# Kernel optimization log

Measured on AMD Instinct MI355X. Metric: run time of the kernel, lower is better.

The kernel has to match this reference:

```python
import jax, jax.numpy as jnp
import numpy as np

B, L, H = 2, 2048, 1536
I, N, R, K = 3072, 16, 96, 4


def setup_inputs() -> dict:
    key = jax.random.key(0)
    ks = jax.random.split(key, 10)
    rn = lambda k, shape, s: jax.random.normal(k, shape, jnp.float32) * s
    return {
        "hidden_states": rn(ks[0], (B, L, H), 1.0),
        "W_in": rn(ks[1], (2 * I, H), 0.02),
        "conv_w": rn(ks[2], (I, K), 0.1),
        "conv_b": rn(ks[3], (I,), 0.1),
        "W_x": rn(ks[4], (R + 2 * N, I), 0.02),
        "W_dt": rn(ks[5], (I, R), 0.02),
        "dt_bias": rn(ks[6], (I,), 0.1),
        # vLLM's weight loader stores A = -exp(A_log); replicate that here
        "A": -jnp.exp(rn(ks[7], (I, N), 0.5)),
        "D": jnp.ones((I,), jnp.float32),
        "W_out": rn(ks[8], (H, I), 0.02),
    }


def reference(hidden_states, W_in, conv_w, conv_b, W_x, W_dt, dt_bias, A, D, W_out):
    b, l, _ = hidden_states.shape
    k = conv_w.shape[1]
    n = A.shape[1]
    r = W_dt.shape[1]

    # in_proj -> [B,L,2I], split into ssm input x and gate
    proj = jnp.einsum("blh,eh->ble", hidden_states, W_in)
    x, gate = jnp.split(proj, 2, axis=-1)  # each [B,L,I]

    # causal depthwise conv1d over L (pad K-1 on the left) + SiLU
    xp = jnp.pad(x, ((0, 0), (k - 1, 0), (0, 0)))
    conv = sum(xp[:, j : j + l, :] * conv_w[:, j] for j in range(k)) + conv_b
    x = jax.nn.silu(conv)  # [B,L,I]

    # x_proj -> dt (rank R), B, C (each N)
    ssm_p = jnp.einsum("bli,pi->blp", x, W_x)
    dt_in, Bm, Cm = jnp.split(ssm_p, [r, r + n], axis=-1)

    # dt_proj (skip_bias_add) then softplus(dt + bias) inside the scan math
    dt = jnp.einsum("blr,ir->bli", dt_in, W_dt)
    delta = jax.nn.softplus(dt + dt_bias)  # [B,L,I]

    # selective scan: s_t = exp(delta_t * A) * s_{t-1} + delta_t * x_t * B_t
    def step(state, inp):
        d_t, u_t, B_t, C_t = inp  # [B,I], [B,I], [B,N], [B,N]
        dA = jnp.exp(d_t[..., None] * A)  # [B,I,N]
        state = state * dA + (d_t * u_t)[..., None] * B_t[:, None, :]
        y = jnp.einsum("bin,bn->bi", state, C_t)
        return state, y

    init = jnp.zeros((b, x.shape[-1], n), jnp.float32)
    _, ys = jax.lax.scan(
        step,
        init,
        (
            delta.transpose(1, 0, 2),
            x.transpose(1, 0, 2),
            Bm.transpose(1, 0, 2),
            Cm.transpose(1, 0, 2),
        ),
    )
    y = ys.transpose(1, 0, 2) + x * D  # skip connection via D
    y = y * jax.nn.silu(gate)

    # out_proj -> [B,L,H]
    return jnp.einsum("bli,hi->blh", y, W_out)
```

## Files before the change

kernel.cpp:

```cpp
#include <hip/hip_runtime.h>

typedef __attribute__((ext_vector_type(8))) short bf16x8;
typedef __attribute__((ext_vector_type(4))) float f32x4;

#define CCH 32
#define TCH 64

__device__ __forceinline__ unsigned short f2b(float f) {
    unsigned u = __float_as_uint(f);
    return (unsigned short)((u + 0x7fffu + ((u >> 16) & 1u)) >> 16);
}
__device__ __forceinline__ float b2f(unsigned short h) {
    return __uint_as_float(((unsigned)h) << 16);
}
__device__ __forceinline__ float softplus_f(float z) {
    return (z > 15.f) ? z : __logf(1.f + __expf(z));
}
__device__ __forceinline__ float silu_f(float g) {
    return g / (1.f + __expf(-g));
}

__device__ __forceinline__ void gload16(const unsigned short* g, unsigned short* l) {
    __builtin_amdgcn_global_load_lds(
        (const __attribute__((address_space(1))) void*)g,
        (__attribute__((address_space(3))) void*)l, 16, 0, 0);
}

__global__ __launch_bounds__(256)
void cast_all(const float* __restrict__ h, const float* __restrict__ win,
              const float* __restrict__ wx, const float* __restrict__ wdt,
              const float* __restrict__ wout,
              unsigned short* __restrict__ dh, unsigned short* __restrict__ dwin,
              unsigned short* __restrict__ dwx, unsigned short* __restrict__ dwdt,
              unsigned short* __restrict__ dwout) {
    const int n0 = 1572864, n1 = n0 + 2359296, n2 = n1 + 98304,
              n3 = n2 + 73728, n4 = n3 + 1179648;
    int i = blockIdx.x * 256 + threadIdx.x;
    const float* s; unsigned short* d; int off;
    if (i < n0)      { s = h;    d = dh;    off = i; }
    else if (i < n1) { s = win;  d = dwin;  off = i - n0; }
    else if (i < n2) { s = wx;   d = dwx;   off = i - n1; }
    else if (i < n3) { s = wdt;  d = dwdt;  off = i - n2; }
    else if (i < n4) { s = wout; d = dwout; off = i - n3; }
    else return;
    float4 v = reinterpret_cast<const float4*>(s)[off];
    ushort4 o;
    o.x = f2b(v.x); o.y = f2b(v.y); o.z = f2b(v.z); o.w = f2b(v.w);
    reinterpret_cast<ushort4*>(d)[off] = o;
}

__global__ __launch_bounds__(768, 3)
void gemm_in(const unsigned short* __restrict__ A, const unsigned short* __restrict__ W,
             unsigned short* __restrict__ Cout, int Kc, int lda, int ldw, int ldc,
             int silu_col0) {
    __shared__ __align__(16) unsigned short A0s[8192];
    __shared__ __align__(16) unsigned short B0s[12288];
    __shared__ __align__(16) unsigned short A1s[8192];
    __shared__ __align__(16) unsigned short B1s[12288];
    const int tid  = threadIdx.x;
    const int lane = tid & 63;
    const int wave = tid >> 6;
    const int wr   = wave / 6;
    const int wcc  = wave % 6;
    const int lr   = lane & 15;
    const int quad = lane >> 4;
    const int sw2  = (lr >> 1) & 3;

    const int c  = blockIdx.x & 7;
    const int j  = blockIdx.x >> 3;
    const int bn = (c * 2 + (j & 1)) * 384;
    const int bm = (j >> 1) * 256;

    const int rsub = wave * 16 + (lane >> 2);
    const int csw  = ((lane & 3) ^ ((lane >> 3) & 3)) * 8;
    const unsigned short* gA = A + (size_t)(bm + rsub) * lda + csw;
    const unsigned short* gB = W + (size_t)(bn + rsub) * ldw + csw;

#define STAGE_A(ARR, kt) do { \
        gload16(gA + (kt) * 32, ARR + wave * 512); \
        if (wave < 4) gload16(gA + (size_t)192 * lda + (kt) * 32, ARR + 6144 + wave * 512); \
    } while (0)
#define STAGE_B(ARR, kt) do { \
        gload16(gB + (kt) * 32, ARR + wave * 512); \
        gload16(gB + (size_t)192 * ldw + (kt) * 32, ARR + 6144 + wave * 512); \
    } while (0)

#define LDA_F(ARR, mi) \
    (*reinterpret_cast<const bf16x8*>(&ARR[(wr * 128 + (mi) * 16 + lr) * 32 + ((quad ^ sw2)) * 8]))
#define LDB_F(ARR, ni) \
    (*reinterpret_cast<const bf16x8*>(&ARR[(wcc * 64 + (ni) * 16 + lr) * 32 + ((quad ^ sw2)) * 8]))

#define PRIO1 __builtin_amdgcn_s_setprio(1)
#define PRIO0 __builtin_amdgcn_s_setprio(0)
#define VM0B  asm volatile("s_waitcnt vmcnt(0)\n\ts_barrier" ::: "memory")

#define TILE_BODY(AX, BX) do { \
        _Pragma("unroll") for (int ni = 0; ni < 4; ++ni) fb[ni] = LDB_F(BX, ni); \
        _Pragma("unroll") for (int mp = 0; mp < 4; ++mp) { \
            bf16x8 fa0 = LDA_F(AX, 2 * mp); \
            bf16x8 fa1 = LDA_F(AX, 2 * mp + 1); \
            PRIO1; \
            _Pragma("unroll") for (int ni = 0; ni < 4; ++ni) { \
                acc[2 * mp][ni]     = __builtin_amdgcn_mfma_f32_16x16x32_bf16(fa0, fb[ni], acc[2 * mp][ni], 0, 0, 0); \
                acc[2 * mp + 1][ni] = __builtin_amdgcn_mfma_f32_16x16x32_bf16(fa1, fb[ni], acc[2 * mp + 1][ni], 0, 0, 0); } \
            PRIO0; } \
    } while (0)

    f32x4 acc[8][4];
    const f32x4 zero = {0.f, 0.f, 0.f, 0.f};
#pragma unroll
    for (int m = 0; m < 8; ++m)
#pragma unroll
        for (int n = 0; n < 4; ++n) acc[m][n] = zero;

    bf16x8 fb[4];

    const int nkt = Kc >> 5;

    STAGE_A(A0s, 0); STAGE_B(B0s, 0);
    VM0B;

#pragma unroll 1
    for (int t = 0; t < nkt; t += 2) {
        if (t + 1 < nkt) { STAGE_A(A1s, t + 1); STAGE_B(B1s, t + 1); }
        TILE_BODY(A0s, B0s);
        VM0B;
        if (t + 1 < nkt) {
            if (t + 2 < nkt) { STAGE_A(A0s, t + 2); STAGE_B(B0s, t + 2); }
            TILE_BODY(A1s, B1s);
            VM0B;
        }
    }

#pragma unroll
    for (int mi = 0; mi < 8; ++mi) {
        const int row0 = bm + wr * 128 + mi * 16 + quad * 4;
#pragma unroll
        for (int ni = 0; ni < 4; ++ni) {
            const int col = bn + wcc * 64 + ni * 16 + lr;
#pragma unroll
            for (int reg = 0; reg < 4; ++reg) {
                float v = acc[mi][ni][reg];
                if (col >= silu_col0) v = silu_f(v);
                Cout[(size_t)(row0 + reg) * ldc + col] = f2b(v);
            }
        }
    }
#undef STAGE_A
#undef STAGE_B
#undef LDA_F
#undef LDB_F
#undef PRIO1
#undef PRIO0
#undef VM0B
#undef TILE_BODY
}

__global__ __launch_bounds__(768, 3)
void gemm_out(const unsigned short* __restrict__ A, const unsigned short* __restrict__ W,
              float* __restrict__ Cout, int Kc, int lda, int ldw, int ldc) {
    __shared__ __align__(16) unsigned short A0s[8192];
    __shared__ __align__(16) unsigned short B0s[12288];
    __shared__ __align__(16) unsigned short A1s[8192];
    __shared__ __align__(16) unsigned short B1s[12288];
    const int tid  = threadIdx.x;
    const int lane = tid & 63;
    const int wave = tid >> 6;
    const int wr   = wave / 6;
    const int wcc  = wave % 6;
    const int lr   = lane & 15;
    const int quad = lane >> 4;
    const int sw   = lr & 7;

    const int c  = blockIdx.x & 7;
    const int j  = blockIdx.x >> 3;
    const int bm = j * 128;
    const int bn = c * 192;

    const int rsub = wave * 8 + (lane >> 3);
    const int csw  = ((lane & 7) ^ ((lane >> 3) & 7)) * 8;
    const unsigned short* gA = A + (size_t)(bm + rsub) * lda + csw;
    const unsigned short* gB = W + (size_t)(bn + rsub) * ldw + csw;

#define STAGE_A(ARR, kt) do { \
        gload16(gA + (kt) * 64, ARR + wave * 512); \
        if (wave < 4) gload16(gA + (size_t)96 * lda + (kt) * 64, ARR + 6144 + wave * 512); \
    } while (0)
#define STAGE_B(ARR, kt) do { \
        gload16(gB + (kt) * 64, ARR + wave * 512); \
        gload16(gB + (size_t)96 * ldw + (kt) * 64, ARR + 6144 + wave * 512); \
    } while (0)

#define LDA_F(ARR, mi, kk) \
    (*reinterpret_cast<const bf16x8*>(&ARR[(wr * 64 + (mi) * 16 + lr) * 64 + (((((kk) << 2) | quad)) ^ sw) * 8]))
#define LDB_F(ARR, ni, kk) \
    (*reinterpret_cast<const bf16x8*>(&ARR[(wcc * 32 + (ni) * 16 + lr) * 64 + (((((kk) << 2) | quad)) ^ sw) * 8]))

#define PRIO1 __builtin_amdgcn_s_setprio(1)
#define PRIO0 __builtin_amdgcn_s_setprio(0)
#define VM0B  asm volatile("s_waitcnt vmcnt(0)\n\ts_barrier" ::: "memory")

#define TILE_BODY(AX, BX) do { \
        _Pragma("unroll") for (int ni = 0; ni < 2; ++ni) { \
            fb[ni][0] = LDB_F(BX, ni, 0); fb[ni][1] = LDB_F(BX, ni, 1); } \
        _Pragma("unroll") for (int mi = 0; mi < 4; ++mi) { \
            fa[mi][0] = LDA_F(AX, mi, 0); fa[mi][1] = LDA_F(AX, mi, 1); } \
        PRIO1; \
        _Pragma("unroll") for (int mi = 0; mi < 4; ++mi) \
        _Pragma("unroll") for (int ni = 0; ni < 2; ++ni) { \
            acc[mi][ni] = __builtin_amdgcn_mfma_f32_16x16x32_bf16(fa[mi][0], fb[ni][0], acc[mi][ni], 0, 0, 0); \
            acc[mi][ni] = __builtin_amdgcn_mfma_f32_16x16x32_bf16(fa[mi][1], fb[ni][1], acc[mi][ni], 0, 0, 0); } \
        PRIO0; \
    } while (0)

    f32x4 acc[4][2];
    const f32x4 zero = {0.f, 0.f, 0.f, 0.f};
#pragma unroll
    for (int m = 0; m < 4; ++m) { acc[m][0] = zero; acc[m][1] = zero; }

    bf16x8 fa[4][2], fb[2][2];

    const int nkt = Kc >> 6;

    STAGE_A(A0s, 0); STAGE_B(B0s, 0);
    VM0B;

#pragma unroll 1
    for (int t = 0; t < nkt; t += 2) {
        if (t + 1 < nkt) { STAGE_A(A1s, t + 1); STAGE_B(B1s, t + 1); }
        TILE_BODY(A0s, B0s);
        VM0B;
        if (t + 1 < nkt) {
            if (t + 2 < nkt) { STAGE_A(A0s, t + 2); STAGE_B(B0s, t + 2); }
            TILE_BODY(A1s, B1s);
            VM0B;
        }
    }

#pragma unroll
    for (int mi = 0; mi < 4; ++mi) {
        const int row0 = bm + wr * 64 + mi * 16 + quad * 4;
#pragma unroll
        for (int ni = 0; ni < 2; ++ni) {
            const int col = bn + wcc * 32 + ni * 16 + lr;
#pragma unroll
            for (int reg = 0; reg < 4; ++reg)
                Cout[(size_t)(row0 + reg) * ldc + col] = acc[mi][ni][reg];
        }
    }
#undef STAGE_A
#undef STAGE_B
#undef LDA_F
#undef LDB_F
#undef PRIO1
#undef PRIO0
#undef VM0B
#undef TILE_BODY
}

template <int OP>
__global__ __launch_bounds__(256)
void gemm_mfma(const unsigned short* __restrict__ A, const unsigned short* __restrict__ W,
               void* __restrict__ Cout, int Kc, int lda, int ldw, int ldc,
               const float* __restrict__ bias, int silu_col0, long long czs) {
    __shared__ unsigned short As[3][4096];
    __shared__ unsigned short Bs[3][4096];
    const int tid = threadIdx.x;
    const int bm = blockIdx.y * 128;
    const int bn = blockIdx.x * 128;
    const int kz = blockIdx.z;
    A += (size_t)kz * Kc;
    W += (size_t)kz * Kc;
    const int lane = tid & 63;
    const int wave = tid >> 6;
    const int r_a = lane >> 2;
    const int k8 = (lane & 3) * 8;

    const unsigned short* gA0 = A + (size_t)(bm + wave * 16 + r_a) * lda + k8;
    const unsigned short* gA1 = A + (size_t)(bm + 64 + wave * 16 + r_a) * lda + k8;
    const unsigned short* gB0 = W + (size_t)(bn + wave * 16 + r_a) * ldw + k8;
    const unsigned short* gB1 = W + (size_t)(bn + 64 + wave * 16 + r_a) * ldw + k8;

    const int wm = (wave & 1) * 64;
    const int wn = (wave >> 1) * 64;
    const int lr = lane & 15;
    const int quad = lane >> 4;

    f32x4 acc[4][4];
    const f32x4 zero = {0.f, 0.f, 0.f, 0.f};
#pragma unroll
    for (int i = 0; i < 4; i++)
#pragma unroll
        for (int j = 0; j < 4; j++) acc[i][j] = zero;

#define STAGE(koff, j) do { \
        gload16(gA0 + (koff), As[j] + wave * 512); \
        gload16(gA1 + (koff), As[j] + (wave + 4) * 512); \
        gload16(gB0 + (koff), Bs[j] + wave * 512); \
        gload16(gB1 + (koff), Bs[j] + (wave + 4) * 512); \
    } while (0)

    const int niter = Kc >> 5;
    STAGE(0, 0);
    if (niter > 1) STAGE(32, 1);

    int ib = 0;
    for (int k = 0; k < niter; k++) {
        if (k + 1 < niter)
            asm volatile("s_waitcnt vmcnt(4)\n\ts_barrier" ::: "memory");
        else
            asm volatile("s_waitcnt vmcnt(0)\n\ts_barrier" ::: "memory");
        if (k + 2 < niter) {
            int is_ = ib + 2; if (is_ >= 3) is_ -= 3;
            STAGE((k + 2) << 5, is_);
        }
        const unsigned short* as = As[ib];
        const unsigned short* bs = Bs[ib];
        bf16x8 fa[4], fb[4];
#pragma unroll
        for (int mi = 0; mi < 4; mi++)
            fa[mi] = *reinterpret_cast<const bf16x8*>(as + (wm + mi * 16 + lr) * 32 + quad * 8);
#pragma unroll
        for (int ni = 0; ni < 4; ni++)
            fb[ni] = *reinterpret_cast<const bf16x8*>(bs + (wn + ni * 16 + lr) * 32 + quad * 8);
#pragma unroll
        for (int mi = 0; mi < 4; mi++)
#pragma unroll
            for (int ni = 0; ni < 4; ni++)
                acc[mi][ni] = __builtin_amdgcn_mfma_f32_16x16x32_bf16(fa[mi], fb[ni], acc[mi][ni], 0, 0, 0);
        ib = (ib == 2) ? 0 : ib + 1;
    }
#undef STAGE

#pragma unroll
    for (int mi = 0; mi < 4; mi++)
#pragma unroll
        for (int reg = 0; reg < 4; reg++) {
            int row = bm + wm + mi * 16 + quad * 4 + reg;
#pragma unroll
            for (int ni = 0; ni < 4; ni++) {
                int col = bn + wn + ni * 16 + lr;
                float v = acc[mi][ni][reg];
                if (OP == 0) {
                    float* Cf = (float*)Cout + (size_t)kz * czs;
                    Cf[(size_t)row * ldc + col] = v;
                } else if (OP == 2) {
                    if (col >= silu_col0) v = silu_f(v);
                    ((unsigned short*)Cout)[(size_t)row * ldc + col] = f2b(v);
                } else {
                    ((unsigned short*)Cout)[(size_t)row * ldc + col] = f2b(softplus_f(v + bias[col]));
                }
            }
        }
}

__global__ __launch_bounds__(256)
void reduce_xpart(const float* __restrict__ xpart, float* __restrict__ ssmp,
                  unsigned short* __restrict__ dtin) {
    const int BL = 4096;
    int idx = blockIdx.x * 256 + threadIdx.x;
    int row = idx >> 5;
    int c4 = (idx & 31) * 4;
    float4 s = {0.f, 0.f, 0.f, 0.f};
#pragma unroll
    for (int z = 0; z < 8; z++) {
        float4 v = *reinterpret_cast<const float4*>(xpart + (size_t)z * BL * 128 + (size_t)row * 128 + c4);
        s.x += v.x; s.y += v.y; s.z += v.z; s.w += v.w;
    }
    *reinterpret_cast<float4*>(ssmp + (size_t)row * 128 + c4) = s;
    if (c4 < 96) {
        ushort4 o;
        o.x = f2b(s.x); o.y = f2b(s.y); o.z = f2b(s.z); o.w = f2b(s.w);
        *reinterpret_cast<ushort4*>(dtin + (size_t)row * 96 + c4) = o;
    }
}

__global__ __launch_bounds__(256)
void conv_silu8(const unsigned short* __restrict__ projbf, const float* __restrict__ cw,
                const float* __restrict__ cb, unsigned short* __restrict__ xc) {
    const int I = 3072, L = 2048, LD = 6144;
    int idx = blockIdx.x * 256 + threadIdx.x;
    int i8 = (idx % (I / 8)) * 8;
    int bl = idx / (I / 8);
    int l = bl & (L - 1);
    float s[8];
    {
        float4 b0 = *reinterpret_cast<const float4*>(cb + i8);
        float4 b1 = *reinterpret_cast<const float4*>(cb + i8 + 4);
        s[0]=b0.x; s[1]=b0.y; s[2]=b0.z; s[3]=b0.w; s[4]=b1.x; s[5]=b1.y; s[6]=b1.z; s[7]=b1.w;
    }
    float w[8][4];
#pragma unroll
    for (int c = 0; c < 8; c++) {
        float4 wr = *reinterpret_cast<const float4*>(cw + (i8 + c) * 4);
        w[c][0]=wr.x; w[c][1]=wr.y; w[c][2]=wr.z; w[c][3]=wr.w;
    }
#pragma unroll
    for (int j = 0; j < 4; j++) {
        if (l + j - 3 >= 0) {
            uint4 r = *reinterpret_cast<const uint4*>(projbf + (size_t)(bl + j - 3) * LD + i8);
            float xv[8];
            xv[0]=b2f((unsigned short)(r.x & 0xffff)); xv[1]=b2f((unsigned short)(r.x >> 16));
            xv[2]=b2f((unsigned short)(r.y & 0xffff)); xv[3]=b2f((unsigned short)(r.y >> 16));
            xv[4]=b2f((unsigned short)(r.z & 0xffff)); xv[5]=b2f((unsigned short)(r.z >> 16));
            xv[6]=b2f((unsigned short)(r.w & 0xffff)); xv[7]=b2f((unsigned short)(r.w >> 16));
#pragma unroll
            for (int c = 0; c < 8; c++) s[c] = fmaf(xv[c], w[c][j], s[c]);
        }
    }
    unsigned short o[8];
#pragma unroll
    for (int c = 0; c < 8; c++) o[c] = f2b(silu_f(s[c]));
    uint4 packed;
    packed.x = (unsigned)o[0] | ((unsigned)o[1] << 16);
    packed.y = (unsigned)o[2] | ((unsigned)o[3] << 16);
    packed.z = (unsigned)o[4] | ((unsigned)o[5] << 16);
    packed.w = (unsigned)o[6] | ((unsigned)o[7] << 16);
    *reinterpret_cast<uint4*>(xc + (size_t)bl * I + i8) = packed;
}

__global__ __launch_bounds__(256)
void scan_passA(const unsigned short* __restrict__ delta_bf, const unsigned short* __restrict__ xc,
                const float* __restrict__ ssmp, const float* __restrict__ Aw,
                float* __restrict__ S_local, float* __restrict__ sumDelta) {
    const int I = 3072, L = 2048;
    __shared__ float bc[TCH][32];
    int g = blockIdx.x * 256 + threadIdx.x;
    int i = g % I;
    int bcid = g / I;
    int c = bcid % CCH;
    int b = bcid / CCH;
    size_t rowbase = (size_t)b * L + (size_t)c * TCH;
    for (int e = threadIdx.x; e < TCH * 8; e += 256) {
        int t = e >> 3, q = e & 7;
        float4 v = *reinterpret_cast<const float4*>(ssmp + (rowbase + t) * 128 + 96 + q * 4);
        *reinterpret_cast<float4*>(&bc[t][q * 4]) = v;
    }
    __syncthreads();

    float Arow[16];
#pragma unroll
    for (int n = 0; n < 16; n++) Arow[n] = Aw[i * 16 + n];
    float st[16];
#pragma unroll
    for (int n = 0; n < 16; n++) st[n] = 0.f;
    float sumD = 0.f;

    size_t rowI = rowbase * I + i;
    for (int t = 0; t < TCH; t++) {
        float delta = b2f(delta_bf[rowI]);
        float du = delta * b2f(xc[rowI]);
        sumD += delta;
        float4 b0 = *reinterpret_cast<const float4*>(&bc[t][0]);
        float4 b1 = *reinterpret_cast<const float4*>(&bc[t][4]);
        float4 b2 = *reinterpret_cast<const float4*>(&bc[t][8]);
        float4 b3 = *reinterpret_cast<const float4*>(&bc[t][12]);
        const float bv[16] = {b0.x,b0.y,b0.z,b0.w, b1.x,b1.y,b1.z,b1.w,
                              b2.x,b2.y,b2.z,b2.w, b3.x,b3.y,b3.z,b3.w};
#pragma unroll
        for (int n = 0; n < 16; n++)
            st[n] = fmaf(st[n], __expf(delta * Arow[n]), du * bv[n]);
        rowI += I;
    }
    size_t obase = (size_t)bcid * 16 * I + i;
#pragma unroll
    for (int n = 0; n < 16; n++) S_local[obase + (size_t)n * I] = st[n];
    sumDelta[(size_t)bcid * I + i] = sumD;
}

__global__ __launch_bounds__(256)
void scan_passB(const float* __restrict__ S_local, const float* __restrict__ sumDelta,
                const float* __restrict__ Aw, float* __restrict__ state_in) {
    const int I = 3072;
    int g = blockIdx.x * 256 + threadIdx.x;
    int i = g % I;
    int bn = g / I;
    int n = bn & 15;
    int b = bn >> 4;
    float a = Aw[i * 16 + n];
    float state = 0.f;
    for (int c = 0; c < CCH; c++) {
        int bcid = b * CCH + c;
        size_t idx = ((size_t)bcid * 16 + n) * I + i;
        state_in[idx] = state;
        state = fmaf(state, __expf(a * sumDelta[(size_t)bcid * I + i]), S_local[idx]);
    }
}

__global__ __launch_bounds__(256)
void scan_passC(const unsigned short* __restrict__ projbf,
                const unsigned short* __restrict__ xc,
                const float* __restrict__ ssmp, const unsigned short* __restrict__ delta_bf,
                const float* __restrict__ Aw, const float* __restrict__ Dw,
                const float* __restrict__ state_in, unsigned short* __restrict__ ybf) {
    const int I = 3072, L = 2048, LD = 6144;
    __shared__ float bc[TCH][32];
    int g = blockIdx.x * 256 + threadIdx.x;
    int i = g % I;
    int bcid = g / I;
    int c = bcid % CCH;
    int b = bcid / CCH;
    size_t rowbase = (size_t)b * L + (size_t)c * TCH;
    for (int e = threadIdx.x; e < TCH * 8; e += 256) {
        int t = e >> 3, q = e & 7;
        float4 v = *reinterpret_cast<const float4*>(ssmp + (rowbase + t) * 128 + 96 + q * 4);
        *reinterpret_cast<float4*>(&bc[t][q * 4]) = v;
    }
    __syncthreads();

    float Arow[16];
#pragma unroll
    for (int n = 0; n < 16; n++) Arow[n] = Aw[i * 16 + n];
    float Dv = Dw[i];
    float st[16];
    size_t sbase = (size_t)bcid * 16 * I + i;
#pragma unroll
    for (int n = 0; n < 16; n++) st[n] = state_in[sbase + (size_t)n * I];

    size_t rowI = rowbase * I + i;
    size_t rowG = rowbase * LD + I + i;
    for (int t = 0; t < TCH; t++) {
        float delta = b2f(delta_bf[rowI]);
        float u = b2f(xc[rowI]);
        float du = delta * u;
        float4 b0 = *reinterpret_cast<const float4*>(&bc[t][0]);
        float4 b1 = *reinterpret_cast<const float4*>(&bc[t][4]);
        float4 b2 = *reinterpret_cast<const float4*>(&bc[t][8]);
        float4 b3 = *reinterpret_cast<const float4*>(&bc[t][12]);
        float4 c0 = *reinterpret_cast<const float4*>(&bc[t][16]);
        float4 c1 = *reinterpret_cast<const float4*>(&bc[t][20]);
        float4 c2 = *reinterpret_cast<const float4*>(&bc[t][24]);
        float4 c3 = *reinterpret_cast<const float4*>(&bc[t][28]);
        const float bv[16] = {b0.x,b0.y,b0.z,b0.w, b1.x,b1.y,b1.z,b1.w,
                              b2.x,b2.y,b2.z,b2.w, b3.x,b3.y,b3.z,b3.w};
        const float cv[16] = {c0.x,c0.y,c0.z,c0.w, c1.x,c1.y,c1.z,c1.w,
                              c2.x,c2.y,c2.z,c2.w, c3.x,c3.y,c3.z,c3.w};
        float y = 0.f;
#pragma unroll
        for (int n = 0; n < 16; n++) {
            st[n] = fmaf(st[n], __expf(delta * Arow[n]), du * bv[n]);
            y = fmaf(st[n], cv[n], y);
        }
        y = fmaf(u, Dv, y);
        y *= b2f(projbf[rowG]);
        ybf[rowI] = f2b(y);
        rowI += I;
        rowG += LD;
    }
}

extern "C" void kernel_launch(void* const* d_in, const int* in_sizes, int n_in,
                              void* d_out, int out_size, void* d_ws, size_t ws_size,
                              hipStream_t stream) {
    const float* hidden  = (const float*)d_in[0];
    const float* W_in    = (const float*)d_in[1];
    const float* conv_w  = (const float*)d_in[2];
    const float* conv_b  = (const float*)d_in[3];
    const float* W_x     = (const float*)d_in[4];
    const float* W_dt    = (const float*)d_in[5];
    const float* dt_bias = (const float*)d_in[6];
    const float* Aw      = (const float*)d_in[7];
    const float* Dw      = (const float*)d_in[8];
    const float* W_out   = (const float*)d_in[9];
    float* out = (float*)d_out;

    constexpr int Bsz = 2, L = 2048, H = 1536, I = 3072, R = 96;
    constexpr int BL = Bsz * L;
    constexpr int TwoI = 2 * I;

    char* base = (char*)d_ws;
    unsigned short* proj_bf  = (unsigned short*)base; base += (size_t)BL * TwoI * 2;
    unsigned short* delta_bf = (unsigned short*)base; base += (size_t)BL * I * 2;
    unsigned short* xc_bf    = (unsigned short*)base; base += (size_t)BL * I * 2;
    unsigned short* y_bf     = (unsigned short*)base; base += (size_t)BL * I * 2;
    float* ssmp              = (float*)base;          base += (size_t)BL * 128 * 4;
    float* xpart             = (float*)base;          base += (size_t)8 * BL * 128 * 4;
    unsigned short* dtin_bf  = (unsigned short*)base; base += (size_t)BL * R * 2;
    unsigned short* wx_bf    = (unsigned short*)base; base += (size_t)128 * I * 2;
    unsigned short* wdt_bf   = (unsigned short*)base; base += (size_t)I * R * 2;
    unsigned short* wout_bf  = (unsigned short*)base; base += (size_t)H * I * 2;
    unsigned short* h_bf     = (unsigned short*)base; base += (size_t)BL * H * 2;
    unsigned short* win_bf   = (unsigned short*)base; base += (size_t)TwoI * H * 2;
    float* S_local  = (float*)h_bf;
    float* sumDelta = S_local + (size_t)Bsz * CCH * 16 * I;
    float* state_in = sumDelta + (size_t)Bsz * CCH * I;

    dim3 blk(256);

    cast_all<<<(5283840 + 255) / 256, blk, 0, stream>>>(
        hidden, W_in, W_x, W_dt, W_out, h_bf, win_bf, wx_bf, wdt_bf, wout_bf);

    gemm_in<<<dim3(256, 1, 1), dim3(768), 0, stream>>>(
        h_bf, win_bf, proj_bf, H, H, H, TwoI,  I);

    conv_silu8<<<BL * I / 8 / 256, blk, 0, stream>>>(proj_bf, conv_w, conv_b, xc_bf);

    gemm_mfma<0><<<dim3(1, BL / 128, 8), blk, 0, stream>>>(
        xc_bf, wx_bf, xpart, I / 8, I, I, 128, nullptr, 0, (long long)BL * 128);
    reduce_xpart<<<BL * 32 / 256, blk, 0, stream>>>(xpart, ssmp, dtin_bf);

    gemm_mfma<3><<<dim3(I / 128, BL / 128, 1), blk, 0, stream>>>(
        dtin_bf, wdt_bf, delta_bf, R, R, R, I, dt_bias, 0, 0);

    scan_passA<<<Bsz * I * CCH / 256, blk, 0, stream>>>(
        delta_bf, xc_bf, ssmp, Aw, S_local, sumDelta);
    scan_passB<<<Bsz * 16 * I / 256, blk, 0, stream>>>(
        S_local, sumDelta, Aw, state_in);
    scan_passC<<<Bsz * I * CCH / 256, blk, 0, stream>>>(
        proj_bf, xc_bf, ssmp, delta_bf, Aw, Dw, state_in, y_bf);

    gemm_out<<<dim3(256, 1, 1), dim3(768), 0, stream>>>(
        y_bf, wout_bf, out, I, I, I, H);
}
```

Baseline: 450.1 us.

## Triple-buffer LDS tiles in in/out projection GEMMs with partial vmcnt waits

Both large bf16 GEMM kernels go from double to triple buffering of the A/B tiles in LDS. The main loop is restructured into three rotating slots, and each slot waits only for the older stage using per-wave vmcnt counts (4 or 3 loads, depending on whether the wave issues the extra A load), instead of draining all loads each iteration. This keeps two tile loads in flight to hide global-memory latency behind MFMA work. In exchange, LDS use per block grows by half, which can reduce how many blocks fit per CU. The loop also always executes three tile bodies per iteration, which assumes the K-tile count is a multiple of three.

```diff
diff --git a/kernel.cpp b/kernel.cpp
--- a/kernel.cpp
+++ b/kernel.cpp
@@ -54,9 +54,11 @@
              unsigned short* __restrict__ Cout, int Kc, int lda, int ldw, int ldc,
              int silu_col0) {
     __shared__ __align__(16) unsigned short A0s[8192];
+    __shared__ __align__(16) unsigned short A1s[8192];
+    __shared__ __align__(16) unsigned short A2s[8192];
     __shared__ __align__(16) unsigned short B0s[12288];
-    __shared__ __align__(16) unsigned short A1s[8192];
     __shared__ __align__(16) unsigned short B1s[12288];
+    __shared__ __align__(16) unsigned short B2s[12288];
     const int tid  = threadIdx.x;
     const int lane = tid & 63;
     const int wave = tid >> 6;
@@ -65,6 +67,7 @@
     const int lr   = lane & 15;
     const int quad = lane >> 4;
     const int sw2  = (lr >> 1) & 3;
+    const int hiAu = __builtin_amdgcn_readfirstlane(wave < 4 ? 1 : 0);
 
     const int c  = blockIdx.x & 7;
     const int j  = blockIdx.x >> 3;
@@ -78,7 +81,7 @@
 
 #define STAGE_A(ARR, kt) do { \
         gload16(gA + (kt) * 32, ARR + wave * 512); \
-        if (wave < 4) gload16(gA + (size_t)192 * lda + (kt) * 32, ARR + 6144 + wave * 512); \
+        if (hiAu) gload16(gA + (size_t)192 * lda + (kt) * 32, ARR + 6144 + wave * 512); \
     } while (0)
 #define STAGE_B(ARR, kt) do { \
         gload16(gB + (kt) * 32, ARR + wave * 512); \
@@ -92,7 +95,11 @@
 
 #define PRIO1 __builtin_amdgcn_s_setprio(1)
 #define PRIO0 __builtin_amdgcn_s_setprio(0)
-#define VM0B  asm volatile("s_waitcnt vmcnt(0)\n\ts_barrier" ::: "memory")
+#define WTB do { \
+        if (hiAu) asm volatile("s_waitcnt vmcnt(4)\n\ts_barrier" ::: "memory"); \
+        else      asm volatile("s_waitcnt vmcnt(3)\n\ts_barrier" ::: "memory"); \
+    } while (0)
+#define VM0B asm volatile("s_waitcnt vmcnt(0)\n\ts_barrier" ::: "memory")
 
 #define TILE_BODY(AX, BX) do { \
         _Pragma("unroll") for (int ni = 0; ni < 4; ++ni) fb[ni] = LDB_F(BX, ni); \
@@ -106,6 +113,14 @@
             PRIO0; } \
     } while (0)
 
+#define SLOT(RA, RB, SA, SB, ts) do { \
+        if ((ts) < nkt) { STAGE_A(SA, ts); STAGE_B(SB, ts); } \
+        TILE_BODY(RA, RB); \
+        if ((ts) < nkt)       WTB; \
+        else if ((ts) == nkt) VM0B; \
+        else asm volatile("s_barrier" ::: "memory"); \
+    } while (0)
+
     f32x4 acc[8][4];
     const f32x4 zero = {0.f, 0.f, 0.f, 0.f};
 #pragma unroll
@@ -118,18 +133,14 @@
     const int nkt = Kc >> 5;
 
     STAGE_A(A0s, 0); STAGE_B(B0s, 0);
-    VM0B;
+    STAGE_A(A1s, 1); STAGE_B(B1s, 1);
+    WTB;
 
 #pragma unroll 1
-    for (int t = 0; t < nkt; t += 2) {
-        if (t + 1 < nkt) { STAGE_A(A1s, t + 1); STAGE_B(B1s, t + 1); }
-        TILE_BODY(A0s, B0s);
-        VM0B;
-        if (t + 1 < nkt) {
-            if (t + 2 < nkt) { STAGE_A(A0s, t + 2); STAGE_B(B0s, t + 2); }
-            TILE_BODY(A1s, B1s);
-            VM0B;
-        }
+    for (int t = 0; t < nkt; t += 3) {
+        SLOT(A0s, B0s, A2s, B2s, t + 2);
+        SLOT(A1s, B1s, A0s, B0s, t + 3);
+        SLOT(A2s, B2s, A1s, B1s, t + 4);
     }
 
 #pragma unroll
@@ -152,17 +163,21 @@
 #undef LDB_F
 #undef PRIO1
 #undef PRIO0
+#undef WTB
 #undef VM0B
 #undef TILE_BODY
+#undef SLOT
 }
 
 __global__ __launch_bounds__(768, 3)
 void gemm_out(const unsigned short* __restrict__ A, const unsigned short* __restrict__ W,
               float* __restrict__ Cout, int Kc, int lda, int ldw, int ldc) {
     __shared__ __align__(16) unsigned short A0s[8192];
+    __shared__ __align__(16) unsigned short A1s[8192];
+    __shared__ __align__(16) unsigned short A2s[8192];
     __shared__ __align__(16) unsigned short B0s[12288];
-    __shared__ __align__(16) unsigned short A1s[8192];
     __shared__ __align__(16) unsigned short B1s[12288];
+    __shared__ __align__(16) unsigned short B2s[12288];
     const int tid  = threadIdx.x;
     const int lane = tid & 63;
     const int wave = tid >> 6;
@@ -171,6 +186,7 @@
     const int lr   = lane & 15;
     const int quad = lane >> 4;
     const int sw   = lr & 7;
+    const int hiAu = __builtin_amdgcn_readfirstlane(wave < 4 ? 1 : 0);
 
     const int c  = blockIdx.x & 7;
     const int j  = blockIdx.x >> 3;
@@ -184,7 +200,7 @@
 
 #define STAGE_A(ARR, kt) do { \
         gload16(gA + (kt) * 64, ARR + wave * 512); \
-        if (wave < 4) gload16(gA + (size_t)96 * lda + (kt) * 64, ARR + 6144 + wave * 512); \
+        if (hiAu) gload16(gA + (size_t)96 * lda + (kt) * 64, ARR + 6144 + wave * 512); \
     } while (0)
 #define STAGE_B(ARR, kt) do { \
         gload16(gB + (kt) * 64, ARR + wave * 512); \
@@ -198,7 +214,11 @@
 
 #define PRIO1 __builtin_amdgcn_s_setprio(1)
 #define PRIO0 __builtin_amdgcn_s_setprio(0)
-#define VM0B  asm volatile("s_waitcnt vmcnt(0)\n\ts_barrier" ::: "memory")
+#define WTB do { \
+        if (hiAu) asm volatile("s_waitcnt vmcnt(4)\n\ts_barrier" ::: "memory"); \
+        else      asm volatile("s_waitcnt vmcnt(3)\n\ts_barrier" ::: "memory"); \
+    } while (0)
+#define VM0B asm volatile("s_waitcnt vmcnt(0)\n\ts_barrier" ::: "memory")
 
 #define TILE_BODY(AX, BX) do { \
         _Pragma("unroll") for (int ni = 0; ni < 2; ++ni) { \
@@ -213,6 +233,14 @@
         PRIO0; \
     } while (0)
 
+#define SLOT(RA, RB, SA, SB, ts) do { \
+        if ((ts) < nkt) { STAGE_A(SA, ts); STAGE_B(SB, ts); } \
+        TILE_BODY(RA, RB); \
+        if ((ts) < nkt)       WTB; \
+        else if ((ts) == nkt) VM0B; \
+        else asm volatile("s_barrier" ::: "memory"); \
+    } while (0)
+
     f32x4 acc[4][2];
     const f32x4 zero = {0.f, 0.f, 0.f, 0.f};
 #pragma unroll
@@ -223,18 +251,14 @@
     const int nkt = Kc >> 6;
 
     STAGE_A(A0s, 0); STAGE_B(B0s, 0);
-    VM0B;
+    STAGE_A(A1s, 1); STAGE_B(B1s, 1);
+    WTB;
 
 #pragma unroll 1
-    for (int t = 0; t < nkt; t += 2) {
-        if (t + 1 < nkt) { STAGE_A(A1s, t + 1); STAGE_B(B1s, t + 1); }
-        TILE_BODY(A0s, B0s);
-        VM0B;
-        if (t + 1 < nkt) {
-            if (t + 2 < nkt) { STAGE_A(A0s, t + 2); STAGE_B(B0s, t + 2); }
-            TILE_BODY(A1s, B1s);
-            VM0B;
-        }
+    for (int t = 0; t < nkt; t += 3) {
+        SLOT(A0s, B0s, A2s, B2s, t + 2);
+        SLOT(A1s, B1s, A0s, B0s, t + 3);
+        SLOT(A2s, B2s, A1s, B1s, t + 4);
     }
 
 #pragma unroll
@@ -254,8 +278,10 @@
 #undef LDB_F
 #undef PRIO1
 #undef PRIO0
+#undef WTB
 #undef VM0B
 #undef TILE_BODY
+#undef SLOT
 }
 
 template <int OP>
```

Result: slower. 474.5 us (+5.4%).

## Triple-buffer the in-projection GEMM LDS pipeline with partial vmcnt waits

Applied to the files above, without the earlier changes.

The in-projection GEMM changes from a double-buffered LDS pipeline to a triple-buffered one. Loads for tile t+2 are issued while tile t is computed, and the wait becomes vmcnt(5), so only the older tile's loads must land before the barrier. Staging is reassigned so 8 of the 12 waves each issue 5 global-to-LDS loads, and the K loop is unrolled by three slots. The goal is to hide global-load latency better. The cost is 50% more LDS per block, which may reduce blocks resident per CU, and four idle waves during staging.

```diff
diff --git a/kernel.cpp b/kernel.cpp
--- a/kernel.cpp
+++ b/kernel.cpp
@@ -54,9 +54,11 @@
              unsigned short* __restrict__ Cout, int Kc, int lda, int ldw, int ldc,
              int silu_col0) {
     __shared__ __align__(16) unsigned short A0s[8192];
+    __shared__ __align__(16) unsigned short A1s[8192];
+    __shared__ __align__(16) unsigned short A2s[8192];
     __shared__ __align__(16) unsigned short B0s[12288];
-    __shared__ __align__(16) unsigned short A1s[8192];
     __shared__ __align__(16) unsigned short B1s[12288];
+    __shared__ __align__(16) unsigned short B2s[12288];
     const int tid  = threadIdx.x;
     const int lane = tid & 63;
     const int wave = tid >> 6;
@@ -71,18 +73,20 @@
     const int bn = (c * 2 + (j & 1)) * 384;
     const int bm = (j >> 1) * 256;
 
-    const int rsub = wave * 16 + (lane >> 2);
     const int csw  = ((lane & 3) ^ ((lane >> 3) & 3)) * 8;
-    const unsigned short* gA = A + (size_t)(bm + rsub) * lda + csw;
-    const unsigned short* gB = W + (size_t)(bn + rsub) * ldw + csw;
-
-#define STAGE_A(ARR, kt) do { \
-        gload16(gA + (kt) * 32, ARR + wave * 512); \
-        if (wave < 4) gload16(gA + (size_t)192 * lda + (kt) * 32, ARR + 6144 + wave * 512); \
-    } while (0)
-#define STAGE_B(ARR, kt) do { \
-        gload16(gB + (kt) * 32, ARR + wave * 512); \
-        gload16(gB + (size_t)192 * ldw + (kt) * 32, ARR + 6144 + wave * 512); \
+    const unsigned short* gAl = A + (size_t)(bm + (lane >> 2)) * lda + csw;
+    const unsigned short* gBl = W + (size_t)(bn + (lane >> 2)) * ldw + csw;
+    const int la0 = wave * 2;
+    const int lb0 = wave * 3;
+
+#define STAGE(AR, BR, kt) do { \
+        if (wave < 8) { \
+            gload16(gAl + (size_t)(16 * la0) * lda + (kt) * 32,          AR + la0 * 512); \
+            gload16(gAl + (size_t)(16 * la0 + 16) * lda + (kt) * 32,     AR + la0 * 512 + 512); \
+            gload16(gBl + (size_t)(16 * lb0) * ldw + (kt) * 32,          BR + lb0 * 512); \
+            gload16(gBl + (size_t)(16 * lb0 + 16) * ldw + (kt) * 32,     BR + lb0 * 512 + 512); \
+            gload16(gBl + (size_t)(16 * lb0 + 32) * ldw + (kt) * 32,     BR + lb0 * 512 + 1024); \
+        } \
     } while (0)
 
 #define LDA_F(ARR, mi) \
@@ -92,7 +96,9 @@
 
 #define PRIO1 __builtin_amdgcn_s_setprio(1)
 #define PRIO0 __builtin_amdgcn_s_setprio(0)
-#define VM0B  asm volatile("s_waitcnt vmcnt(0)\n\ts_barrier" ::: "memory")
+#define WTB  asm volatile("s_waitcnt vmcnt(5)\n\ts_barrier" ::: "memory")
+#define VM0B asm volatile("s_waitcnt vmcnt(0)\n\ts_barrier" ::: "memory")
+#define BARO asm volatile("s_barrier" ::: "memory")
 
 #define TILE_BODY(AX, BX) do { \
         _Pragma("unroll") for (int ni = 0; ni < 4; ++ni) fb[ni] = LDB_F(BX, ni); \
@@ -106,6 +112,14 @@
             PRIO0; } \
     } while (0)
 
+#define SLOT(RA, RB, SA, SB, ts) do { \
+        if ((ts) < nkt) STAGE(SA, SB, ts); \
+        TILE_BODY(RA, RB); \
+        if ((ts) < nkt)       WTB; \
+        else if ((ts) == nkt) VM0B; \
+        else                  BARO; \
+    } while (0)
+
     f32x4 acc[8][4];
     const f32x4 zero = {0.f, 0.f, 0.f, 0.f};
 #pragma unroll
@@ -117,19 +131,15 @@
 
     const int nkt = Kc >> 5;
 
-    STAGE_A(A0s, 0); STAGE_B(B0s, 0);
-    VM0B;
+    STAGE(A0s, B0s, 0);
+    STAGE(A1s, B1s, 1);
+    WTB;
 
 #pragma unroll 1
-    for (int t = 0; t < nkt; t += 2) {
-        if (t + 1 < nkt) { STAGE_A(A1s, t + 1); STAGE_B(B1s, t + 1); }
-        TILE_BODY(A0s, B0s);
-        VM0B;
-        if (t + 1 < nkt) {
-            if (t + 2 < nkt) { STAGE_A(A0s, t + 2); STAGE_B(B0s, t + 2); }
-            TILE_BODY(A1s, B1s);
-            VM0B;
-        }
+    for (int t = 0; t < nkt; t += 3) {
+        SLOT(A0s, B0s, A2s, B2s, t + 2);
+        SLOT(A1s, B1s, A0s, B0s, t + 3);
+        SLOT(A2s, B2s, A1s, B1s, t + 4);
     }
 
 #pragma unroll
@@ -146,14 +156,16 @@
             }
         }
     }
-#undef STAGE_A
-#undef STAGE_B
+#undef STAGE
 #undef LDA_F
 #undef LDB_F
 #undef PRIO1
 #undef PRIO0
+#undef WTB
 #undef VM0B
+#undef BARO
 #undef TILE_BODY
+#undef SLOT
 }
 
 __global__ __launch_bounds__(768, 3)
```

Result: slower. 531.4 us (+18.1%).
